# Kernel optimization log

Hardware: AMD Instinct MI355X
Metric: run time of the kernel (lower is better)

Reference implementation:

```python
import jax, jax.numpy as jnp
import numpy as np


def setup_inputs() -> dict:
    key = jax.random.key(0)
    k1, k2 = jax.random.split(key)
    N, K, C = 2, 32, 32
    h, w = 64, 64
    H, W = 1024, 1024
    grid = jax.random.normal(k1, (N, K, C, h, w), dtype=jnp.float32)
    guidemap = jax.random.normal(k2, (N, C, H, W), dtype=jnp.float32)
    return {"grid": grid, "guidemap": guidemap}


def reference(grid, guidemap):
    N, C, H, W = guidemap.shape
    h, w = grid.shape[3], grid.shape[4]
    f1, f2 = H // h, W // w
    # F.unfold with kernel==stride (non-overlapping blocks):
    # [N,C,H,W] -> [N,C,f1*f2,h,w] with kernel elements row-major within a block.
    g = guidemap.reshape(N, C, h, f1, w, f2)
    g = g.transpose(0, 1, 3, 5, 2, 4).reshape(N, C, f1 * f2, h, w)
    # Per-location small contraction over channels C.
    out = jnp.einsum('ikjmn,ijlmn->iklmn', grid, g)  # [N,K,f1*f2,h,w]
    # F.fold with kernel==stride (non-overlapping scatter, no overlap-add):
    out = out.reshape(N, -1, f1, f2, h, w)
    out = out.transpose(0, 1, 4, 2, 5, 3).reshape(N, -1, H, W)
    return out
```

## Files before the change

### kernel.cpp

```cpp
#include <hip/hip_runtime.h>


namespace {
constexpr int K = 32, C = 32;
constexpr int W = 1024;
constexpr int HW = 1024 * 1024;
constexpr size_t GRDN = (size_t)K * C * 64 * 64;
}

__device__ __forceinline__ void gl_lds4(const float* src, float* dst) {
    __builtin_amdgcn_global_load_lds(
        (const __attribute__((address_space(1))) void*)src,
        (__attribute__((address_space(3))) void*)dst, 4, 0, 0);
}

__global__ __launch_bounds__(256, 4) void gridup_kernel(
    const float* __restrict__ grd,
    const float* __restrict__ gm,
    float* __restrict__ out)
{
    __shared__ float sM[2][C][K];

    int wg = blockIdx.x;
    wg = (wg & 7) * 512 + (wg >> 3);
    const int t = threadIdx.x;
    const int g0 = wg * 2;

    #pragma unroll
    for (int i = 0; i < 8; ++i) {
        const int e  = i * 256 + t;
        const int t2 = e >> 10;
        const int c  = (e >> 5) & 31;
        const int k  = e & 31;
        const int gt2 = g0 + t2;
        const int n2  = gt2 >> 12;
        const int rr2 = gt2 & 4095;
        const int by2 = rr2 >> 6;
        const int bx2 = rr2 & 63;
        gl_lds4(grd + (size_t)n2 * GRDN + (size_t)(k * 32 + c) * 4096 + by2 * 64 + bx2,
                &sM[0][0][0] + e);
    }
    __syncthreads();

    const int tl = t >> 7;
    const int gt = g0 + tl;
    const int n  = gt >> 12;
    const int rr = gt & 4095;
    const int by = rr >> 6;
    const int bx = rr & 63;

    const float* M = &sM[tl][0][0];
    const int p   = (t & 127) * 2;
    const int row = p >> 4;
    const int col = p & 15;
    const size_t pix = (size_t)(by * 16 + row) * W + bx * 16 + col;
    const float* gb = gm + (size_t)n * C * HW + pix;
    float*       ob = out + (size_t)n * K * HW + pix;

    float acc[32][2] = {};
    float2 gc[4], gn[4];
    #pragma unroll
    for (int j = 0; j < 4; ++j)
        gc[j] = *reinterpret_cast<const float2*>(gb + (size_t)j * HW);

    for (int cb = 0; cb < 8; ++cb) {
        if (cb < 7) {
            #pragma unroll
            for (int j = 0; j < 4; ++j)
                gn[j] = *reinterpret_cast<const float2*>(
                    gb + (size_t)((cb + 1) * 4 + j) * HW);
        }
        #pragma unroll
        for (int j = 0; j < 4; ++j) {
            const int c = cb * 4 + j;
            const float2 g = gc[j];
            #pragma unroll
            for (int kq = 0; kq < 8; ++kq) {
                const float4 m = *reinterpret_cast<const float4*>(M + c * 32 + kq * 4);
                acc[kq * 4 + 0][0] += m.x * g.x;  acc[kq * 4 + 0][1] += m.x * g.y;
                acc[kq * 4 + 1][0] += m.y * g.x;  acc[kq * 4 + 1][1] += m.y * g.y;
                acc[kq * 4 + 2][0] += m.z * g.x;  acc[kq * 4 + 2][1] += m.z * g.y;
                acc[kq * 4 + 3][0] += m.w * g.x;  acc[kq * 4 + 3][1] += m.w * g.y;
            }
        }
        if (cb < 7) {
            #pragma unroll
            for (int j = 0; j < 4; ++j) gc[j] = gn[j];
        }
    }

    #pragma unroll
    for (int k = 0; k < 32; ++k) {
        const float2 v = {acc[k][0], acc[k][1]};
        *reinterpret_cast<float2*>(ob + (size_t)k * HW) = v;
    }
}

extern "C" void kernel_launch(void* const* d_in, const int* in_sizes, int n_in,
                              void* d_out, int out_size, void* d_ws, size_t ws_size,
                              hipStream_t stream) {
    const float* grd = (const float*)d_in[0];
    const float* gm  = (const float*)d_in[1];
    float* out = (float*)d_out;

    gridup_kernel<<<4096, 256, 0, stream>>>(grd, gm, out);
}
```

Before: 165.2 us.

## Pre-transpose grid into workspace and stream coefficients via scalar loads

Adds a pre-pass kernel that transposes each block's 32x32 grid matrix into a contiguous workspace, then a main kernel where each wave reads its 16 output channels' coefficients with s_load_dwordx16 into SGPRs instead of LDS. Each lane now computes 4 pixels with float4 guide loads and stores, and channel loads are software-pipelined. This removes LDS traffic and the strided gather from the main loop, at the cost of an extra kernel launch and a 32 MB workspace round trip. A fallback path keeps the old kernel when the workspace is too small.

```diff
diff --git a/kernel.cpp b/kernel.cpp
--- a/kernel.cpp
+++ b/kernel.cpp
@@ -1,4 +1,5 @@
 #include <hip/hip_runtime.h>
+#include <stdint.h>
 
 
 namespace {
@@ -6,6 +7,109 @@
 constexpr int W = 1024;
 constexpr int HW = 1024 * 1024;
 constexpr size_t GRDN = (size_t)K * C * 64 * 64;
+constexpr size_t WS_BYTES = (size_t)8192 * 1024 * 4;
+}
+
+typedef float f32x16 __attribute__((ext_vector_type(16)));
+
+__global__ __launch_bounds__(256) void mat_transpose_kernel(
+    const float* __restrict__ grd, float* __restrict__ ws)
+{
+    int wg = blockIdx.x;
+    wg = (wg & 7) * 1024 + (wg >> 3);
+    const int t = threadIdx.x;
+    const int n  = wg >> 12;
+    const int rr = wg & 4095;
+    const int by = rr >> 6, bx = rr & 63;
+    const float* g = grd + (size_t)n * GRDN + by * 64 + bx;
+    const int e0 = t * 4;
+    const int c  = e0 >> 5;
+    const int k0 = e0 & 31;
+    float4 v;
+    v.x = g[(size_t)((k0 + 0) * 32 + c) * 4096];
+    v.y = g[(size_t)((k0 + 1) * 32 + c) * 4096];
+    v.z = g[(size_t)((k0 + 2) * 32 + c) * 4096];
+    v.w = g[(size_t)((k0 + 3) * 32 + c) * 4096];
+    *reinterpret_cast<float4*>(ws + (size_t)wg * 1024 + e0) = v;
+}
+
+__global__ __launch_bounds__(256, 4) void gridup_main(
+    const float* __restrict__ ws,
+    const float* __restrict__ gm,
+    float* __restrict__ out)
+{
+    const int b  = blockIdx.x;
+    const int wg = (b & 7) * 512 + (b >> 3);
+    const int t  = threadIdx.x;
+    const int w  = t >> 6;
+    const int tl = w >> 1;
+    const int kh = w & 1;
+    const int l  = t & 63;
+
+    const int gt = wg * 2 + tl;
+    const int n  = gt >> 12;
+    const int rr = gt & 4095;
+    const int by = rr >> 6, bx = rr & 63;
+
+    const int row = l >> 2, col4 = (l & 3) << 2;
+    const size_t pix = (size_t)(by * 16 + row) * W + bx * 16 + col4;
+    const float* gb = gm + (size_t)n * C * HW + pix;
+    float* ob = out + ((size_t)n * K + kh * 16) * HW + pix;
+
+    const uint64_t a = (uint64_t)(ws + (size_t)gt * 1024 + kh * 16);
+    const uint32_t alo = __builtin_amdgcn_readfirstlane((uint32_t)a);
+    const uint32_t ahi = __builtin_amdgcn_readfirstlane((uint32_t)(a >> 32));
+    const uint64_t mp = ((uint64_t)ahi << 32) | alo;
+
+    f32x16 mA, mB;
+    asm volatile("s_load_dwordx16 %0, %2, 0\n\t"
+                 "s_load_dwordx16 %1, %2, 128"
+                 : "=s"(mA), "=s"(mB)
+                 : "s"(mp));
+
+    float4 g[4];
+#pragma unroll
+    for (int j = 0; j < 4; ++j)
+        g[j] = *reinterpret_cast<const float4*>(gb + (size_t)j * HW);
+
+    float acc[16][4] = {};
+
+#pragma unroll
+    for (int cp = 0; cp < 16; ++cp) {
+        asm volatile("s_waitcnt lgkmcnt(0)" : "+s"(mA), "+s"(mB) :: "memory");
+        const f32x16 fA = mA, fB = mB;
+        if (cp < 15) {
+            asm volatile("s_load_dwordx16 %0, %2, %3\n\t"
+                         "s_load_dwordx16 %1, %2, %4"
+                         : "=s"(mA), "=s"(mB)
+                         : "s"(mp), "i"((2 * cp + 2) * 128),
+                                    "i"((2 * cp + 3) * 128));
+        }
+        const float4 gv0 = g[(2 * cp) & 3];
+        const float4 gv1 = g[(2 * cp + 1) & 3];
+        if (2 * cp + 4 < 32)
+            g[(2 * cp) & 3] = *reinterpret_cast<const float4*>(
+                gb + (size_t)(2 * cp + 4) * HW);
+        if (2 * cp + 5 < 32)
+            g[(2 * cp + 1) & 3] = *reinterpret_cast<const float4*>(
+                gb + (size_t)(2 * cp + 5) * HW);
+#pragma unroll
+        for (int k = 0; k < 16; ++k) {
+            acc[k][0] += fA[k] * gv0.x;  acc[k][1] += fA[k] * gv0.y;
+            acc[k][2] += fA[k] * gv0.z;  acc[k][3] += fA[k] * gv0.w;
+        }
+#pragma unroll
+        for (int k = 0; k < 16; ++k) {
+            acc[k][0] += fB[k] * gv1.x;  acc[k][1] += fB[k] * gv1.y;
+            acc[k][2] += fB[k] * gv1.z;  acc[k][3] += fB[k] * gv1.w;
+        }
+    }
+
+#pragma unroll
+    for (int k = 0; k < 16; ++k) {
+        const float4 v = {acc[k][0], acc[k][1], acc[k][2], acc[k][3]};
+        *reinterpret_cast<float4*>(ob + (size_t)k * HW) = v;
+    }
 }
 
 __device__ __forceinline__ void gl_lds4(const float* src, float* dst) {
@@ -14,82 +118,64 @@
         (__attribute__((address_space(3))) void*)dst, 4, 0, 0);
 }
 
-__global__ __launch_bounds__(256, 4) void gridup_kernel(
-    const float* __restrict__ grd,
-    const float* __restrict__ gm,
+__global__ __launch_bounds__(256, 4) void gridup_fb(
+    const float* __restrict__ grd, const float* __restrict__ gm,
     float* __restrict__ out)
 {
     __shared__ float sM[2][C][K];
-
     int wg = blockIdx.x;
     wg = (wg & 7) * 512 + (wg >> 3);
     const int t = threadIdx.x;
     const int g0 = wg * 2;
-
-    #pragma unroll
+#pragma unroll
     for (int i = 0; i < 8; ++i) {
-        const int e  = i * 256 + t;
-        const int t2 = e >> 10;
-        const int c  = (e >> 5) & 31;
-        const int k  = e & 31;
-        const int gt2 = g0 + t2;
-        const int n2  = gt2 >> 12;
-        const int rr2 = gt2 & 4095;
-        const int by2 = rr2 >> 6;
-        const int bx2 = rr2 & 63;
-        gl_lds4(grd + (size_t)n2 * GRDN + (size_t)(k * 32 + c) * 4096 + by2 * 64 + bx2,
+        const int e = i * 256 + t;
+        const int t2 = e >> 10, c = (e >> 5) & 31, k = e & 31;
+        const int gt2 = g0 + t2, n2 = gt2 >> 12, rr2 = gt2 & 4095;
+        gl_lds4(grd + (size_t)n2 * GRDN + (size_t)(k * 32 + c) * 4096 +
+                    (rr2 >> 6) * 64 + (rr2 & 63),
                 &sM[0][0][0] + e);
     }
     __syncthreads();
-
     const int tl = t >> 7;
-    const int gt = g0 + tl;
-    const int n  = gt >> 12;
-    const int rr = gt & 4095;
-    const int by = rr >> 6;
-    const int bx = rr & 63;
-
+    const int gt = g0 + tl, n = gt >> 12, rr = gt & 4095;
+    const int by = rr >> 6, bx = rr & 63;
     const float* M = &sM[tl][0][0];
-    const int p   = (t & 127) * 2;
-    const int row = p >> 4;
-    const int col = p & 15;
+    const int p = (t & 127) * 2, row = p >> 4, col = p & 15;
     const size_t pix = (size_t)(by * 16 + row) * W + bx * 16 + col;
     const float* gb = gm + (size_t)n * C * HW + pix;
-    float*       ob = out + (size_t)n * K * HW + pix;
-
+    float* ob = out + (size_t)n * K * HW + pix;
     float acc[32][2] = {};
     float2 gc[4], gn[4];
-    #pragma unroll
+#pragma unroll
     for (int j = 0; j < 4; ++j)
         gc[j] = *reinterpret_cast<const float2*>(gb + (size_t)j * HW);
-
     for (int cb = 0; cb < 8; ++cb) {
         if (cb < 7) {
-            #pragma unroll
+#pragma unroll
             for (int j = 0; j < 4; ++j)
                 gn[j] = *reinterpret_cast<const float2*>(
                     gb + (size_t)((cb + 1) * 4 + j) * HW);
         }
-        #pragma unroll
+#pragma unroll
         for (int j = 0; j < 4; ++j) {
             const int c = cb * 4 + j;
-            const float2 g = gc[j];
-            #pragma unroll
+            const float2 gv = gc[j];
+#pragma unroll
             for (int kq = 0; kq < 8; ++kq) {
                 const float4 m = *reinterpret_cast<const float4*>(M + c * 32 + kq * 4);
-                acc[kq * 4 + 0][0] += m.x * g.x;  acc[kq * 4 + 0][1] += m.x * g.y;
-                acc[kq * 4 + 1][0] += m.y * g.x;  acc[kq * 4 + 1][1] += m.y * g.y;
-                acc[kq * 4 + 2][0] += m.z * g.x;  acc[kq * 4 + 2][1] += m.z * g.y;
-                acc[kq * 4 + 3][0] += m.w * g.x;  acc[kq * 4 + 3][1] += m.w * g.y;
+                acc[kq * 4 + 0][0] += m.x * gv.x; acc[kq * 4 + 0][1] += m.x * gv.y;
+                acc[kq * 4 + 1][0] += m.y * gv.x; acc[kq * 4 + 1][1] += m.y * gv.y;
+                acc[kq * 4 + 2][0] += m.z * gv.x; acc[kq * 4 + 2][1] += m.z * gv.y;
+                acc[kq * 4 + 3][0] += m.w * gv.x; acc[kq * 4 + 3][1] += m.w * gv.y;
             }
         }
         if (cb < 7) {
-            #pragma unroll
+#pragma unroll
             for (int j = 0; j < 4; ++j) gc[j] = gn[j];
         }
     }
-
-    #pragma unroll
+#pragma unroll
     for (int k = 0; k < 32; ++k) {
         const float2 v = {acc[k][0], acc[k][1]};
         *reinterpret_cast<float2*>(ob + (size_t)k * HW) = v;
@@ -103,5 +189,11 @@
     const float* gm  = (const float*)d_in[1];
     float* out = (float*)d_out;
 
-    gridup_kernel<<<4096, 256, 0, stream>>>(grd, gm, out);
+    if (ws_size >= WS_BYTES) {
+        float* ws = (float*)d_ws;
+        mat_transpose_kernel<<<8192, 256, 0, stream>>>(grd, ws);
+        gridup_main<<<4096, 256, 0, stream>>>(ws, gm, out);
+    } else {
+        gridup_fb<<<4096, 256, 0, stream>>>(grd, gm, out);
+    }
 }
```

Result: slower. 210.0 us (+27.1%).

## Remap threads to 4 pixels x 16 outputs with float4 loads and stores

Applied to the files above, without the earlier changes.

Changes the thread-to-work mapping so each thread computes 4 contiguous pixels for half of the K outputs, instead of 2 pixels for all 32 outputs. The two blocks a workgroup handles are now horizontally adjacent, and each wave covers either the top or bottom 8 rows of both. Guidemap reads and output writes become float4, and the channel loop keeps a rolling 4-deep prefetch. The goal is wider memory transactions and fewer LDS matrix reads per FMA. In exchange, every guidemap value is now loaded twice, once by each K-half wave.

```diff
diff --git a/kernel.cpp b/kernel.cpp
--- a/kernel.cpp
+++ b/kernel.cpp
@@ -21,78 +21,73 @@
 {
     __shared__ float sM[2][C][K];
 
-    int wg = blockIdx.x;
-    wg = (wg & 7) * 512 + (wg >> 3);
-    const int t = threadIdx.x;
-    const int g0 = wg * 2;
+    const int b  = blockIdx.x;
+    const int tp = (b & 7) * 512 + (b >> 3);
+    const int t  = threadIdx.x;
+
+    const int gt0 = tp * 2;
+    const int n   = gt0 >> 12;
+    const int rr  = gt0 & 4095;
+    const int by  = rr >> 6;
+    const int bx0 = rr & 63;
 
     #pragma unroll
     for (int i = 0; i < 8; ++i) {
-        const int e  = i * 256 + t;
-        const int t2 = e >> 10;
-        const int c  = (e >> 5) & 31;
-        const int k  = e & 31;
-        const int gt2 = g0 + t2;
-        const int n2  = gt2 >> 12;
-        const int rr2 = gt2 & 4095;
-        const int by2 = rr2 >> 6;
-        const int bx2 = rr2 & 63;
-        gl_lds4(grd + (size_t)n2 * GRDN + (size_t)(k * 32 + c) * 4096 + by2 * 64 + bx2,
+        const int e   = i * 256 + t;
+        const int bxp = e >> 10;
+        const int c   = (e >> 5) & 31;
+        const int k   = e & 31;
+        gl_lds4(grd + (size_t)n * GRDN + (size_t)(k * 32 + c) * 4096 +
+                    by * 64 + bx0 + bxp,
                 &sM[0][0][0] + e);
     }
     __syncthreads();
 
-    const int tl = t >> 7;
-    const int gt = g0 + tl;
-    const int n  = gt >> 12;
-    const int rr = gt & 4095;
-    const int by = rr >> 6;
-    const int bx = rr & 63;
+    const int l  = t & 63;
+    const int w  = t >> 6;
+    const int rh = w & 1;
+    const int kh = w >> 1;
 
-    const float* M = &sM[tl][0][0];
-    const int p   = (t & 127) * 2;
-    const int row = p >> 4;
-    const int col = p & 15;
-    const size_t pix = (size_t)(by * 16 + row) * W + bx * 16 + col;
-    const float* gb = gm + (size_t)n * C * HW + pix;
-    float*       ob = out + (size_t)n * K * HW + pix;
+    const int r    = l >> 3;
+    const int bxp  = (l >> 2) & 1;
+    const int cq   = l & 3;
 
-    float acc[32][2] = {};
-    float2 gc[4], gn[4];
+    const int row   = by * 16 + rh * 8 + r;
+    const int colpx = (bx0 + bxp) * 16 + cq * 4;
+    const float* gb = gm + (size_t)n * C * HW + (size_t)row * W + colpx;
+    float*       ob = out + ((size_t)n * K + kh * 16) * HW + (size_t)row * W + colpx;
+    const float* Mb = &sM[bxp][0][kh * 16];
+
+    float4 g[4];
     #pragma unroll
     for (int j = 0; j < 4; ++j)
-        gc[j] = *reinterpret_cast<const float2*>(gb + (size_t)j * HW);
+        g[j] = *reinterpret_cast<const float4*>(gb + (size_t)j * HW);
 
-    for (int cb = 0; cb < 8; ++cb) {
-        if (cb < 7) {
-            #pragma unroll
-            for (int j = 0; j < 4; ++j)
-                gn[j] = *reinterpret_cast<const float2*>(
-                    gb + (size_t)((cb + 1) * 4 + j) * HW);
-        }
+    float acc[16][4] = {};
+
+    #pragma unroll
+    for (int c = 0; c < C; ++c) {
+        const float4 gv = g[c & 3];
+        if (c + 4 < C)
+            g[c & 3] = *reinterpret_cast<const float4*>(gb + (size_t)(c + 4) * HW);
         #pragma unroll
-        for (int j = 0; j < 4; ++j) {
-            const int c = cb * 4 + j;
-            const float2 g = gc[j];
-            #pragma unroll
-            for (int kq = 0; kq < 8; ++kq) {
-                const float4 m = *reinterpret_cast<const float4*>(M + c * 32 + kq * 4);
-                acc[kq * 4 + 0][0] += m.x * g.x;  acc[kq * 4 + 0][1] += m.x * g.y;
-                acc[kq * 4 + 1][0] += m.y * g.x;  acc[kq * 4 + 1][1] += m.y * g.y;
-                acc[kq * 4 + 2][0] += m.z * g.x;  acc[kq * 4 + 2][1] += m.z * g.y;
-                acc[kq * 4 + 3][0] += m.w * g.x;  acc[kq * 4 + 3][1] += m.w * g.y;
-            }
-        }
-        if (cb < 7) {
-            #pragma unroll
-            for (int j = 0; j < 4; ++j) gc[j] = gn[j];
+        for (int kq = 0; kq < 4; ++kq) {
+            const float4 m = *reinterpret_cast<const float4*>(Mb + c * K + kq * 4);
+            acc[kq * 4 + 0][0] += m.x * gv.x;  acc[kq * 4 + 0][1] += m.x * gv.y;
+            acc[kq * 4 + 0][2] += m.x * gv.z;  acc[kq * 4 + 0][3] += m.x * gv.w;
+            acc[kq * 4 + 1][0] += m.y * gv.x;  acc[kq * 4 + 1][1] += m.y * gv.y;
+            acc[kq * 4 + 1][2] += m.y * gv.z;  acc[kq * 4 + 1][3] += m.y * gv.w;
+            acc[kq * 4 + 2][0] += m.z * gv.x;  acc[kq * 4 + 2][1] += m.z * gv.y;
+            acc[kq * 4 + 2][2] += m.z * gv.z;  acc[kq * 4 + 2][3] += m.z * gv.w;
+            acc[kq * 4 + 3][0] += m.w * gv.x;  acc[kq * 4 + 3][1] += m.w * gv.y;
+            acc[kq * 4 + 3][2] += m.w * gv.z;  acc[kq * 4 + 3][3] += m.w * gv.w;
         }
     }
 
     #pragma unroll
-    for (int k = 0; k < 32; ++k) {
-        const float2 v = {acc[k][0], acc[k][1]};
-        *reinterpret_cast<float2*>(ob + (size_t)k * HW) = v;
+    for (int k = 0; k < 16; ++k) {
+        const float4 v = {acc[k][0], acc[k][1], acc[k][2], acc[k][3]};
+        *reinterpret_cast<float4*>(ob + (size_t)k * HW) = v;
     }
 }
 
```

New measurement: 208.6 us. 26.3% more time.
